# Kernel tuning notes

Hardware: AMD Instinct MI355X
Metric: run time of the kernel (lower is better)

## Reference

```python
import jax, jax.numpy as jnp
import numpy as np

N_NODES = 100000
N_EDGES = 600000
N_ETYPES = 4
IN_DIM = 128
OUT_DIM = 128
N_STEPS = 8
N_GRAPHS = 128


def setup_inputs() -> dict:
    key = jax.random.key(0)
    ks = jax.random.split(key, 12)
    features = jax.random.normal(ks[0], (N_NODES, IN_DIM), dtype=jnp.float32)
    edge_src = jax.random.randint(ks[1], (N_EDGES,), 0, N_NODES, dtype=jnp.int32)
    edge_dst = jax.random.randint(ks[2], (N_EDGES,), 0, N_NODES, dtype=jnp.int32)
    edge_types = jax.random.randint(ks[3], (N_EDGES,), 0, N_ETYPES, dtype=jnp.int32)
    graph_ids = jnp.sort(jax.random.randint(ks[4], (N_NODES,), 0, N_GRAPHS, dtype=jnp.int32))
    s = 1.0 / np.sqrt(OUT_DIM)
    W_edge = jax.random.uniform(ks[5], (N_ETYPES, OUT_DIM, OUT_DIM), jnp.float32, -s, s)
    W_ih = jax.random.uniform(ks[6], (3 * OUT_DIM, OUT_DIM), jnp.float32, -s, s)
    W_hh = jax.random.uniform(ks[7], (3 * OUT_DIM, OUT_DIM), jnp.float32, -s, s)
    b_ih = jax.random.uniform(ks[8], (3 * OUT_DIM,), jnp.float32, -s, s)
    b_hh = jax.random.uniform(ks[9], (3 * OUT_DIM,), jnp.float32, -s, s)
    W_cls = jax.random.uniform(ks[10], (1, OUT_DIM), jnp.float32, -s, s)
    b_cls = jax.random.uniform(ks[11], (1,), jnp.float32, -s, s)
    return dict(features=features, edge_src=edge_src, edge_dst=edge_dst,
                edge_types=edge_types, graph_ids=graph_ids, W_edge=W_edge,
                W_ih=W_ih, W_hh=W_hh, b_ih=b_ih, b_hh=b_hh, W_cls=W_cls, b_cls=b_cls)


def _gru_cell(x, h, W_ih, W_hh, b_ih, b_hh):
    gi = x @ W_ih.T + b_ih  # [N, 3*out]
    gh = h @ W_hh.T + b_hh
    i_r, i_z, i_n = jnp.split(gi, 3, axis=-1)
    h_r, h_z, h_n = jnp.split(gh, 3, axis=-1)
    r = jax.nn.sigmoid(i_r + h_r)
    z = jax.nn.sigmoid(i_z + h_z)
    n = jnp.tanh(i_n + r * h_n)
    return (1.0 - z) * n + z * h


def reference(features, edge_src, edge_dst, edge_types, graph_ids,
              W_edge, W_ih, W_hh, b_ih, b_hh, W_cls, b_cls):
    n_nodes = features.shape[0]
    out_dim = W_edge.shape[-1]
    # DGL GatedGraphConv zero-pads features to out_feats
    pad = out_dim - features.shape[1]
    h = jnp.pad(features, ((0, 0), (0, pad))) if pad > 0 else features

    def step(h, _):
        # per-edge-type linear transform of all nodes: [etype, N, out]
        ht = jnp.einsum('nd,edh->enh', h, W_edge)
        m = ht[edge_types, edge_src]  # gather per-edge messages [E, out]
        a = jax.ops.segment_sum(m, edge_dst, num_segments=n_nodes)
        return _gru_cell(a, h, W_ih, W_hh, b_ih, b_hh), None

    h, _ = jax.lax.scan(step, h, None, length=N_STEPS)
    # de-batchify + sum over nodes per graph == segment_sum over graph ids
    pooled = jax.ops.segment_sum(h, graph_ids, num_segments=N_GRAPHS)  # [B, out]
    logits = pooled @ W_cls.T + b_cls  # [B, 1]
    return jax.nn.sigmoid(logits).squeeze(-1)  # [B]
```

## Files before the change

kernel.cpp:

```cpp
#include <hip/hip_runtime.h>
#include <cstdint>

#define NNODES 100000
#define NEDGES 600000
#define NETYPES 4
#define DIM 128
#define NSTEPS 8
#define NGRAPHS 128
#define NBINS (NETYPES * NNODES)
#define SCAN_BLK 391
#define NTILES (NNODES / 32)
#define PGRID 512
#define GRU_GRID 512

typedef short s16x8 __attribute__((ext_vector_type(8)));
typedef float f32x4 __attribute__((ext_vector_type(4)));

#define MFMA(a, b, c) __builtin_amdgcn_mfma_f32_16x16x32_bf16(a, b, c, 0, 0, 0)

static __device__ inline unsigned short f2bf(float x) {
  unsigned int u = __float_as_uint(x);
  unsigned int r = (u + 0x7FFFu + ((u >> 16) & 1u)) >> 16;
  return (unsigned short)r;
}
static __device__ inline float bf2f(unsigned short b) {
  return __uint_as_float(((unsigned int)b) << 16);
}

__global__ __launch_bounds__(128) void fill_kernel(float* __restrict__ out, int n, float v) {
  int i = blockIdx.x * 128 + threadIdx.x;
  if (i < n) out[i] = v;
}

__global__ __launch_bounds__(256) void cvt_h_kernel(const float* __restrict__ f,
                                                    unsigned short* __restrict__ h, int n4) {
  int i = blockIdx.x * 256 + threadIdx.x;
  if (i < n4) {
    float4 v = ((const float4*)f)[i];
    ushort4 u = {f2bf(v.x), f2bf(v.y), f2bf(v.z), f2bf(v.w)};
    ((ushort4*)h)[i] = u;
  }
}

__global__ __launch_bounds__(256) void cvt_we_kernel(const float* __restrict__ W,
                                                     unsigned short* __restrict__ WT) {
  int i = blockIdx.x * 256 + threadIdx.x;
  if (i < NETYPES * DIM * DIM) {
    int e = i >> 14;
    int r = i & 16383;
    int d = r >> 7;
    int j = r & 127;
    WT[(e << 14) + (j << 7) + d] = f2bf(W[i]);
  }
}

__global__ __launch_bounds__(256) void cvt_w_kernel(const float* __restrict__ W,
                                                    unsigned short* __restrict__ Wb, int n) {
  int i = blockIdx.x * 256 + threadIdx.x;
  if (i < n) Wb[i] = f2bf(W[i]);
}

__global__ __launch_bounds__(256) void hist_kernel(const int* __restrict__ edst,
                                                   const int* __restrict__ etyp,
                                                   int* __restrict__ bins) {
  int e = blockIdx.x * 256 + threadIdx.x;
  if (e < NEDGES) atomicAdd(&bins[etyp[e] * NNODES + edst[e]], 1);
}

__global__ __launch_bounds__(256) void scan1_kernel(const int* __restrict__ bins,
                                                    int* __restrict__ rp,
                                                    int* __restrict__ bsum) {
  __shared__ int sh[256];
  int b = blockIdx.x, t = threadIdx.x;
  int base = b * 1024 + t * 4;
  int v0 = 0, v1 = 0, v2 = 0, v3 = 0;
  if (base + 3 < NBINS) {
    int4 q = *(const int4*)(bins + base);
    v0 = q.x; v1 = q.y; v2 = q.z; v3 = q.w;
  } else {
    if (base < NBINS) v0 = bins[base];
    if (base + 1 < NBINS) v1 = bins[base + 1];
    if (base + 2 < NBINS) v2 = bins[base + 2];
  }
  int s = v0 + v1 + v2 + v3;
  sh[t] = s;
  __syncthreads();
  for (int off = 1; off < 256; off <<= 1) {
    int x = (t >= off) ? sh[t - off] : 0;
    __syncthreads();
    if (t >= off) sh[t] += x;
    __syncthreads();
  }
  int run = sh[t] - s;
  if (t == 255) bsum[b] = sh[255];
  if (base < NBINS) rp[base] = run;
  run += v0;
  if (base + 1 < NBINS) rp[base + 1] = run;
  run += v1;
  if (base + 2 < NBINS) rp[base + 2] = run;
  run += v2;
  if (base + 3 < NBINS) rp[base + 3] = run;
}

__global__ __launch_bounds__(512) void scan2_kernel(const int* __restrict__ bsum,
                                                    int* __restrict__ boffs,
                                                    int* __restrict__ rp) {
  __shared__ int sh[512];
  int t = threadIdx.x;
  int v = (t < SCAN_BLK) ? bsum[t] : 0;
  sh[t] = v;
  __syncthreads();
  for (int off = 1; off < 512; off <<= 1) {
    int x = (t >= off) ? sh[t - off] : 0;
    __syncthreads();
    if (t >= off) sh[t] += x;
    __syncthreads();
  }
  if (t < SCAN_BLK) boffs[t] = sh[t] - v;
  if (t == SCAN_BLK - 1) rp[NBINS] = sh[t];
}

__global__ __launch_bounds__(256) void scan3_kernel(int* __restrict__ rp,
                                                    const int* __restrict__ boffs) {
  int b = blockIdx.x, t = threadIdx.x;
  int base = b * 1024 + t * 4;
  int off = boffs[b];
#pragma unroll
  for (int i = 0; i < 4; ++i)
    if (base + i < NBINS) rp[base + i] += off;
}

__global__ __launch_bounds__(256) void fill_edges_kernel(const int* __restrict__ esrc,
                                                         const int* __restrict__ edst,
                                                         const int* __restrict__ etyp,
                                                         int* __restrict__ cursor,
                                                         int* __restrict__ esrc_s) {
  int e = blockIdx.x * 256 + threadIdx.x;
  if (e < NEDGES) {
    int slot = atomicAdd(&cursor[etyp[e] * NNODES + edst[e]], 1);
    esrc_s[slot] = esrc[e];
  }
}

__global__ __launch_bounds__(256) void agg4_ilv_kernel(const unsigned short* __restrict__ hbf,
                                                       const int* __restrict__ rp,
                                                       const int* __restrict__ esrc_s,
                                                       unsigned short* __restrict__ agg4) {
  int w = (blockIdx.x * 256 + threadIdx.x) >> 6;
  int lane = threadIdx.x & 63;
  if (w >= NNODES) return;
  int beg[4], len[4];
#pragma unroll
  for (int ty = 0; ty < 4; ++ty) {
    beg[ty] = rp[ty * NNODES + w];
    len[ty] = rp[ty * NNODES + w + 1] - beg[ty];
  }
  int mx = max(max(len[0], len[1]), max(len[2], len[3]));
  float ax[4] = {0.f, 0.f, 0.f, 0.f}, ay[4] = {0.f, 0.f, 0.f, 0.f};
#pragma unroll 2
  for (int i = 0; i < mx; ++i) {
#pragma unroll
    for (int ty = 0; ty < 4; ++ty) {
      if (i < len[ty]) {
        int s = esrc_s[beg[ty] + i];
        ushort2 u = *(const ushort2*)(hbf + (size_t)s * DIM + lane * 2);
        ax[ty] += bf2f(u.x);
        ay[ty] += bf2f(u.y);
      }
    }
  }
#pragma unroll
  for (int ty = 0; ty < 4; ++ty) {
    unsigned int packed = ((unsigned int)f2bf(ay[ty]) << 16) | (unsigned int)f2bf(ax[ty]);
    __builtin_nontemporal_store(
        packed, (unsigned int*)(agg4 + (size_t)ty * NNODES * DIM + (size_t)w * DIM + lane * 2));
  }
}

__global__ __launch_bounds__(512, 2) void transform_kernel(const unsigned short* __restrict__ agg4,
                                                           const unsigned short* __restrict__ WeT,
                                                           unsigned short* __restrict__ abf) {
  __shared__ s16x8 lds[2][2048];
  const int t = threadIdx.x;
  const int wid = t >> 6, lane = t & 63;
  const int l15 = lane & 15, kg = lane >> 4;
  const int j0 = wid * 16, jb = j0 + kg * 4;

  s16x8 wf[4][4];
#pragma unroll
  for (int ty = 0; ty < 4; ++ty)
#pragma unroll
    for (int c = 0; c < 4; ++c)
      wf[ty][c] = *(const s16x8*)(WeT + (ty << 14) + ((j0 + l15) << 7) + c * 32 + kg * 8);

  int chk[4], lby[4];
#pragma unroll
  for (int i = 0; i < 4; ++i) {
    chk[i] = t + i * 512;
    int row = (chk[i] & 511) >> 4;
    int w16 = chk[i] & 15;
    lby[i] = (chk[i] >> 9) * 8192 + row * 256 + ((w16 ^ (row & 7)) << 4);
  }
  auto gsrc = [&](int i, int tile) -> const s16x8* {
    int ty = chk[i] >> 9;
    int row = (chk[i] & 511) >> 4;
    int w16 = chk[i] & 15;
    return (const s16x8*)(agg4 + (size_t)ty * NNODES * DIM +
                          (size_t)(tile * 32 + row) * DIM + w16 * 8);
  };

  int tile = blockIdx.x;
  if (tile >= NTILES) return;
  s16x8 st[4];
#pragma unroll
  for (int i = 0; i < 4; ++i) st[i] = __builtin_nontemporal_load(gsrc(i, tile));
#pragma unroll
  for (int i = 0; i < 4; ++i) *(s16x8*)((char*)&lds[0][0] + lby[i]) = st[i];
  int nx = tile + gridDim.x;
  bool hasnx = nx < NTILES;
  if (hasnx)
#pragma unroll
    for (int i = 0; i < 4; ++i) st[i] = __builtin_nontemporal_load(gsrc(i, nx));
  __syncthreads();
  int cur = 0;

  while (true) {
    if (hasnx) {
#pragma unroll
      for (int i = 0; i < 4; ++i) *(s16x8*)((char*)&lds[cur ^ 1][0] + lby[i]) = st[i];
    }
    int nx2 = nx + gridDim.x;
    bool has2 = hasnx && (nx2 < NTILES);
    if (has2) {
#pragma unroll
      for (int i = 0; i < 4; ++i) st[i] = __builtin_nontemporal_load(gsrc(i, nx2));
    }

    f32x4 acc[2] = {(f32x4){0.f, 0.f, 0.f, 0.f}, (f32x4){0.f, 0.f, 0.f, 0.f}};
    char* B0 = (char*)&lds[cur][0];
#pragma unroll
    for (int ty = 0; ty < 4; ++ty) {
#pragma unroll
      for (int c = 0; c < 4; ++c) {
        s16x8 afr[2];
#pragma unroll
        for (int nb = 0; nb < 2; ++nb) {
          int row = nb * 16 + l15;
          afr[nb] = *(const s16x8*)(B0 + ty * 8192 + row * 256 +
                                    ((c * 64 + kg * 16) ^ ((row & 7) << 4)));
        }
        acc[0] = MFMA(wf[ty][c], afr[0], acc[0]);
        acc[1] = MFMA(wf[ty][c], afr[1], acc[1]);
      }
    }
    const int n0 = tile * 32;
#pragma unroll
    for (int nb = 0; nb < 2; ++nb) {
      int n = n0 + nb * 16 + l15;
      ushort4 u = {f2bf(acc[nb][0]), f2bf(acc[nb][1]), f2bf(acc[nb][2]), f2bf(acc[nb][3])};
      *(ushort4*)(abf + (size_t)n * DIM + jb) = u;
    }
    __syncthreads();
    if (!hasnx) break;
    tile = nx;
    nx = nx2;
    hasnx = has2;
    cur ^= 1;
  }
}

__global__ __launch_bounds__(512, 2) void gru_mfma_kernel(const unsigned short* __restrict__ abf,
                                                          unsigned short* __restrict__ hbf,
                                                          const unsigned short* __restrict__ Wih,
                                                          const unsigned short* __restrict__ Whh,
                                                          const float* __restrict__ b_ih,
                                                          const float* __restrict__ b_hh) {
  __shared__ s16x8 lds[2][1024];
  const int t = threadIdx.x;
  const int wid = t >> 6, lane = t & 63;
  const int l15 = lane & 15, kg = lane >> 4;
  const int j0 = wid * 16, jb = j0 + kg * 4;

  s16x8 wI[3][4], wH[3][4];
#pragma unroll
  for (int g = 0; g < 3; ++g)
#pragma unroll
    for (int c = 0; c < 4; ++c) {
      int jrow = g * 128 + j0 + l15;
      wI[g][c] = *(const s16x8*)(Wih + (jrow << 7) + c * 32 + kg * 8);
      wH[g][c] = *(const s16x8*)(Whh + (jrow << 7) + c * 32 + kg * 8);
    }
  float4 bir = *(const float4*)(b_ih + jb);
  float4 biz = *(const float4*)(b_ih + 128 + jb);
  float4 bin_ = *(const float4*)(b_ih + 256 + jb);
  float4 bhr = *(const float4*)(b_hh + jb);
  float4 bhz = *(const float4*)(b_hh + 128 + jb);
  float4 bhn = *(const float4*)(b_hh + 256 + jb);

  int chk0 = t, chk1 = t + 512;
  int row0 = (chk0 & 511) >> 4, w160 = chk0 & 15;
  int row1 = (chk1 & 511) >> 4, w161 = chk1 & 15;
  int lb0 = (chk0 >> 9) * 8192 + row0 * 256 + ((w160 ^ (row0 & 7)) << 4);
  int lb1 = (chk1 >> 9) * 8192 + row1 * 256 + ((w161 ^ (row1 & 7)) << 4);
  int hbyte_lo = (jb * 2) & 15;
  int hbyte_slot = (jb * 2) >> 4;

  int tile = blockIdx.x;
  if (tile >= NTILES) return;
  s16x8 st0, st1;
  st0 = *(const s16x8*)(((chk0 >> 9) ? hbf : abf) + (size_t)(tile * 32 + row0) * DIM + w160 * 8);
  st1 = *(const s16x8*)(((chk1 >> 9) ? hbf : abf) + (size_t)(tile * 32 + row1) * DIM + w161 * 8);
  *(s16x8*)((char*)&lds[0][0] + lb0) = st0;
  *(s16x8*)((char*)&lds[0][0] + lb1) = st1;
  int nx = tile + gridDim.x;
  bool hasnx = nx < NTILES;
  if (hasnx) {
    st0 = *(const s16x8*)(((chk0 >> 9) ? hbf : abf) + (size_t)(nx * 32 + row0) * DIM + w160 * 8);
    st1 = *(const s16x8*)(((chk1 >> 9) ? hbf : abf) + (size_t)(nx * 32 + row1) * DIM + w161 * 8);
  }
  __syncthreads();
  int cur = 0;

  while (true) {
    if (hasnx) {
      *(s16x8*)((char*)&lds[cur ^ 1][0] + lb0) = st0;
      *(s16x8*)((char*)&lds[cur ^ 1][0] + lb1) = st1;
    }
    int nx2 = nx + gridDim.x;
    bool has2 = hasnx && (nx2 < NTILES);
    if (has2) {
      st0 = *(const s16x8*)(((chk0 >> 9) ? hbf : abf) + (size_t)(nx2 * 32 + row0) * DIM + w160 * 8);
      st1 = *(const s16x8*)(((chk1 >> 9) ? hbf : abf) + (size_t)(nx2 * 32 + row1) * DIM + w161 * 8);
    }

    f32x4 gi[3][2], gh[3][2];
#pragma unroll
    for (int g = 0; g < 3; ++g)
#pragma unroll
      for (int nb = 0; nb < 2; ++nb) {
        gi[g][nb] = (f32x4){0.f, 0.f, 0.f, 0.f};
        gh[g][nb] = (f32x4){0.f, 0.f, 0.f, 0.f};
      }
    char* aB = (char*)&lds[cur][0];
    char* hB = aB + 8192;
#pragma unroll
    for (int c = 0; c < 4; ++c) {
      s16x8 afr[2], hfr[2];
#pragma unroll
      for (int nb = 0; nb < 2; ++nb) {
        int row = nb * 16 + l15;
        int off = row * 256 + ((c * 64 + kg * 16) ^ ((row & 7) << 4));
        afr[nb] = *(const s16x8*)(aB + off);
        hfr[nb] = *(const s16x8*)(hB + off);
      }
#pragma unroll
      for (int g = 0; g < 3; ++g) {
        gi[g][0] = MFMA(wI[g][c], afr[0], gi[g][0]);
        gi[g][1] = MFMA(wI[g][c], afr[1], gi[g][1]);
        gh[g][0] = MFMA(wH[g][c], hfr[0], gh[g][0]);
        gh[g][1] = MFMA(wH[g][c], hfr[1], gh[g][1]);
      }
    }

    const int n0 = tile * 32;
#pragma unroll
    for (int nb = 0; nb < 2; ++nb) {
      int row = nb * 16 + l15;
      int n = n0 + row;
      int hb = row * 256 + ((hbyte_slot << 4) ^ ((row & 7) << 4)) + hbyte_lo;
      ushort4 hold4 = *(const ushort4*)(hB + hb);
      ushort4 outu;
#pragma unroll
      for (int reg = 0; reg < 4; ++reg) {
        float ir = gi[0][nb][reg] + ((const float*)&bir)[reg];
        float iz = gi[1][nb][reg] + ((const float*)&biz)[reg];
        float in_ = gi[2][nb][reg] + ((const float*)&bin_)[reg];
        float hr = gh[0][nb][reg] + ((const float*)&bhr)[reg];
        float hz = gh[1][nb][reg] + ((const float*)&bhz)[reg];
        float hn = gh[2][nb][reg] + ((const float*)&bhn)[reg];
        float r = 1.f / (1.f + __expf(-(ir + hr)));
        float z = 1.f / (1.f + __expf(-(iz + hz)));
        float x = in_ + r * hn;
        float ex = __expf(2.f * x);
        float nn = 1.f - 2.f / (ex + 1.f);
        float ho = bf2f(((const unsigned short*)&hold4)[reg]);
        float hv = (1.f - z) * nn + z * ho;
        ((unsigned short*)&outu)[reg] = f2bf(hv);
      }
      *(ushort4*)(hbf + (size_t)n * DIM + jb) = outu;
    }
    __syncthreads();
    if (!hasnx) break;
    tile = nx;
    nx = nx2;
    hasnx = has2;
    cur ^= 1;
  }
}

__global__ __launch_bounds__(128) void pool_kernel(const unsigned short* __restrict__ h,
                                                   const int* __restrict__ gid,
                                                   float* __restrict__ pooled) {
  int j = threadIdx.x;
  int n0 = blockIdx.x * 32;
  int end = n0 + 32;
  if (end > NNODES) end = NNODES;
  int cur = gid[n0];
  float acc = 0.f;
  for (int n = n0; n < end; ++n) {
    int g = gid[n];
    if (g != cur) {
      atomicAdd(&pooled[cur * DIM + j], acc);
      acc = 0.f;
      cur = g;
    }
    acc += bf2f(h[(size_t)n * DIM + j]);
  }
  atomicAdd(&pooled[cur * DIM + j], acc);
}

__global__ __launch_bounds__(128) void cls_kernel(const float* __restrict__ pooled,
                                                  const float* __restrict__ Wc,
                                                  const float* __restrict__ bc,
                                                  float* __restrict__ out) {
  int g = threadIdx.x;
  float acc = bc[0];
  for (int k = 0; k < DIM; ++k) acc = fmaf(pooled[g * DIM + k], Wc[k], acc);
  out[g] = 1.f / (1.f + __expf(-acc));
}

extern "C" void kernel_launch(void* const* d_in, const int* in_sizes, int n_in,
                              void* d_out, int out_size, void* d_ws, size_t ws_size,
                              hipStream_t stream) {
  const float* features = (const float*)d_in[0];
  const int* esrc = (const int*)d_in[1];
  const int* edst = (const int*)d_in[2];
  const int* etyp = (const int*)d_in[3];
  const int* gids = (const int*)d_in[4];
  const float* W_edge = (const float*)d_in[5];
  const float* W_ih = (const float*)d_in[6];
  const float* W_hh = (const float*)d_in[7];
  const float* b_ih = (const float*)d_in[8];
  const float* b_hh = (const float*)d_in[9];
  const float* W_cls = (const float*)d_in[10];
  const float* b_cls = (const float*)d_in[11];
  float* out = (float*)d_out;

  const size_t nd = (size_t)NNODES * DIM;
  char* p = (char*)d_ws;
  auto take = [&](size_t bytes) {
    char* q = p;
    p += (bytes + 15) & ~(size_t)15;
    return (void*)q;
  };
  unsigned short* agg4 = (unsigned short*)take(NETYPES * nd * 2);
  unsigned short* abf = (unsigned short*)take(nd * 2);
  unsigned short* hbf = (unsigned short*)take(nd * 2);
  unsigned short* WeT = (unsigned short*)take(NETYPES * DIM * DIM * 2);
  unsigned short* Wihb = (unsigned short*)take(384 * DIM * 2);
  unsigned short* Whhb = (unsigned short*)take(384 * DIM * 2);
  int* rp = (int*)take((NBINS + 1) * 4);
  int* cursor = (int*)take(NBINS * 4);
  int* bsum = (int*)take(512 * 4);
  int* boffs = (int*)take(512 * 4);
  int* esrc_s = (int*)take(NEDGES * 4);
  float* pooled = (float*)take(NGRAPHS * DIM * 4);
  size_t need = (size_t)(p - (char*)d_ws);

  if (ws_size < need) {
    fill_kernel<<<(out_size + 127) / 128, 128, 0, stream>>>(out, out_size, 0.5f);
    return;
  }

  cvt_h_kernel<<<(int)(nd / 4 + 255) / 256, 256, 0, stream>>>(features, hbf, (int)(nd / 4));
  cvt_we_kernel<<<(NETYPES * DIM * DIM + 255) / 256, 256, 0, stream>>>(W_edge, WeT);
  cvt_w_kernel<<<(384 * DIM + 255) / 256, 256, 0, stream>>>(W_ih, Wihb, 384 * DIM);
  cvt_w_kernel<<<(384 * DIM + 255) / 256, 256, 0, stream>>>(W_hh, Whhb, 384 * DIM);

  hipMemsetAsync(cursor, 0, (size_t)NBINS * 4, stream);
  hist_kernel<<<(NEDGES + 255) / 256, 256, 0, stream>>>(edst, etyp, cursor);
  scan1_kernel<<<SCAN_BLK, 256, 0, stream>>>(cursor, rp, bsum);
  scan2_kernel<<<1, 512, 0, stream>>>(bsum, boffs, rp);
  scan3_kernel<<<SCAN_BLK, 256, 0, stream>>>(rp, boffs);
  hipMemcpyAsync(cursor, rp, (size_t)NBINS * 4, hipMemcpyDeviceToDevice, stream);
  fill_edges_kernel<<<(NEDGES + 255) / 256, 256, 0, stream>>>(esrc, edst, etyp, cursor, esrc_s);

  for (int s = 0; s < NSTEPS; ++s) {
    agg4_ilv_kernel<<<(NNODES * 64 + 255) / 256, 256, 0, stream>>>(hbf, rp, esrc_s, agg4);
    transform_kernel<<<PGRID, 512, 0, stream>>>(agg4, WeT, abf);
    gru_mfma_kernel<<<GRU_GRID, 512, 0, stream>>>(abf, hbf, Wihb, Whhb, b_ih, b_hh);
  }

  hipMemsetAsync(pooled, 0, (size_t)NGRAPHS * DIM * 4, stream);
  pool_kernel<<<(NNODES + 31) / 32, 128, 0, stream>>>(hbf, gids, pooled);
  cls_kernel<<<1, 128, 0, stream>>>(pooled, W_cls, b_cls, out);
}
```

Before: 1.351 ms.

## Fuse edge aggregation and edge-type transform into one kernel on alternate steps

```diff
diff --git a/kernel.cpp b/kernel.cpp
--- a/kernel.cpp
+++ b/kernel.cpp
@@ -266,6 +266,84 @@
     nx = nx2;
     hasnx = has2;
     cur ^= 1;
+  }
+}
+
+__global__ __launch_bounds__(512, 4) void msg2_kernel(const unsigned short* __restrict__ hbf,
+                                                      const int* __restrict__ rp,
+                                                      const int* __restrict__ esrc_s,
+                                                      const unsigned short* __restrict__ WeT,
+                                                      unsigned short* __restrict__ abf) {
+  __shared__ char lds[32768];
+  const int t = threadIdx.x;
+  const int wid = t >> 6, lane = t & 63;
+  const int l15 = lane & 15, kg = lane >> 4;
+  const int j0 = wid * 16, jb = j0 + kg * 4;
+  const int swz_w = lane >> 2;
+  const int sub = (lane & 3) * 4;
+
+  for (int tile = blockIdx.x; tile < NTILES; tile += gridDim.x) {
+    const int n0 = tile * 32;
+#pragma unroll
+    for (int pass = 0; pass < 2; ++pass) {
+      int beg[8], len[8];
+#pragma unroll
+      for (int s = 0; s < 8; ++s) {
+        int node = n0 + wid * 4 + pass * 2 + (s >> 2);
+        int idx = (s & 3) * NNODES + node;
+        beg[s] = rp[idx];
+        len[s] = rp[idx + 1] - beg[s];
+      }
+      int mx = 0;
+#pragma unroll
+      for (int s = 0; s < 8; ++s) mx = max(mx, len[s]);
+      float ax[8] = {0.f, 0.f, 0.f, 0.f, 0.f, 0.f, 0.f, 0.f};
+      float ay[8] = {0.f, 0.f, 0.f, 0.f, 0.f, 0.f, 0.f, 0.f};
+      for (int i = 0; i < mx; ++i) {
+#pragma unroll
+        for (int s = 0; s < 8; ++s) {
+          if (i < len[s]) {
+            int src = esrc_s[beg[s] + i];
+            ushort2 u = *(const ushort2*)(hbf + (size_t)src * DIM + lane * 2);
+            ax[s] += bf2f(u.x);
+            ay[s] += bf2f(u.y);
+          }
+        }
+      }
+#pragma unroll
+      for (int s = 0; s < 8; ++s) {
+        int row = wid * 4 + pass * 2 + (s >> 2);
+        int lbase = row * 256 + ((swz_w ^ (row & 7)) << 4) + sub;
+        unsigned int packed = ((unsigned int)f2bf(ay[s]) << 16) | (unsigned int)f2bf(ax[s]);
+        *(unsigned int*)(lds + (s & 3) * 8192 + lbase) = packed;
+      }
+    }
+    __syncthreads();
+
+    f32x4 acc[2] = {(f32x4){0.f, 0.f, 0.f, 0.f}, (f32x4){0.f, 0.f, 0.f, 0.f}};
+#pragma unroll
+    for (int ty = 0; ty < 4; ++ty) {
+#pragma unroll
+      for (int c = 0; c < 4; ++c) {
+        s16x8 wfr = *(const s16x8*)(WeT + (ty << 14) + ((j0 + l15) << 7) + c * 32 + kg * 8);
+        s16x8 afr[2];
+#pragma unroll
+        for (int nb = 0; nb < 2; ++nb) {
+          int row = nb * 16 + l15;
+          afr[nb] = *(const s16x8*)(lds + ty * 8192 + row * 256 +
+                                    ((c * 64 + kg * 16) ^ ((row & 7) << 4)));
+        }
+        acc[0] = MFMA(wfr, afr[0], acc[0]);
+        acc[1] = MFMA(wfr, afr[1], acc[1]);
+      }
+    }
+#pragma unroll
+    for (int nb = 0; nb < 2; ++nb) {
+      int n = n0 + nb * 16 + l15;
+      ushort4 u = {f2bf(acc[nb][0]), f2bf(acc[nb][1]), f2bf(acc[nb][2]), f2bf(acc[nb][3])};
+      *(ushort4*)(abf + (size_t)n * DIM + jb) = u;
+    }
+    __syncthreads();
   }
 }
 
@@ -486,8 +564,12 @@
   fill_edges_kernel<<<(NEDGES + 255) / 256, 256, 0, stream>>>(esrc, edst, etyp, cursor, esrc_s);
 
   for (int s = 0; s < NSTEPS; ++s) {
-    agg4_ilv_kernel<<<(NNODES * 64 + 255) / 256, 256, 0, stream>>>(hbf, rp, esrc_s, agg4);
-    transform_kernel<<<PGRID, 512, 0, stream>>>(agg4, WeT, abf);
+    if ((s & 1) == 0) {
+      msg2_kernel<<<PGRID, 512, 0, stream>>>(hbf, rp, esrc_s, WeT, abf);
+    } else {
+      agg4_ilv_kernel<<<(NNODES * 64 + 255) / 256, 256, 0, stream>>>(hbf, rp, esrc_s, agg4);
+      transform_kernel<<<PGRID, 512, 0, stream>>>(agg4, WeT, abf);
+    }
     gru_mfma_kernel<<<GRU_GRID, 512, 0, stream>>>(abf, hbf, Wihb, Whhb, b_ih, b_hh);
   }
 
```

New measurement: 1.528 ms. +13.1%, slower.
